# Kernel tuning notes

Hardware: AMD Instinct MI355X
Metric: run time of the kernel (lower is better)

Reference implementation:

```python
import jax, jax.numpy as jnp
import numpy as np

N = 20000      # points
K = 16         # neighbor pairs per query per branch
M = N * K      # total pairs
C = 384        # embed_dim
H = 6          # num_heads
HD = C // H    # head_dim = 64
H1 = H // 2    # cartesian-branch heads
L = 24         # quant_grid_length (window 6.0 / quant 0.25)
Q = 0.25       # quant_size
LS = 24        # quant_grid_length_sphere (120 / 5)
QS = 5.0       # quant_size_sphere
A = 0.05 * 0.25  # exponential_split 'a'
SCALE = HD ** -0.5


def setup_inputs() -> dict:
    key = jax.random.key(0)
    ks = jax.random.split(key, 12)
    s = 0.02
    inp = {}
    inp["query_feats"] = jax.random.normal(ks[0], (N, C), jnp.float32)
    inp["xyz"] = jax.random.uniform(ks[1], (N, 3), jnp.float32, -3.0, 3.0)
    inp["index_0"] = jnp.repeat(jnp.arange(N, dtype=jnp.int32), K)
    inp["index_1"] = jax.random.randint(ks[2], (M,), 0, N, dtype=jnp.int32)
    inp["index_0_sphere"] = jnp.repeat(jnp.arange(N, dtype=jnp.int32), K)
    inp["index_1_sphere"] = jax.random.randint(ks[3], (M,), 0, N, dtype=jnp.int32)
    inp["W_qkv"] = jax.random.normal(ks[4], (C, 3 * C), jnp.float32) * s
    inp["b_qkv"] = jnp.zeros((3 * C,), jnp.float32)
    inp["W_proj"] = jax.random.normal(ks[5], (C, C), jnp.float32) * s
    inp["b_proj"] = jnp.zeros((C,), jnp.float32)
    inp["tq"] = jax.random.normal(ks[6], (2 * L - 1, 3, H1, HD), jnp.float32) * s
    inp["tk"] = jax.random.normal(ks[7], (2 * L - 1, 3, H1, HD), jnp.float32) * s
    inp["tv"] = jax.random.normal(ks[8], (2 * L - 1, 3, H1, HD), jnp.float32) * s
    inp["tq_s"] = jax.random.normal(ks[9], (2 * LS, 3, H - H1, HD), jnp.float32) * s
    inp["tk_s"] = jax.random.normal(ks[10], (2 * LS, 3, H - H1, HD), jnp.float32) * s
    inp["tv_s"] = jax.random.normal(ks[11], (2 * LS, 3, H - H1, HD), jnp.float32) * s
    return inp


def _cart2sphere(xyz):
    x, y, z = xyz[:, 0], xyz[:, 1], xyz[:, 2]
    theta = (jnp.arctan2(y, x) + np.pi) * (180.0 / np.pi)
    beta = jnp.arctan2(jnp.sqrt(x * x + y * y), z) * (180.0 / np.pi)
    r = jnp.sqrt(x * x + y * y + z * z)
    return jnp.stack([theta, beta, r], -1)


def _rel_idx_cart(xyz, i0, i1):
    rel = xyz[i0] - xyz[i1]  # [M,3]
    idx = jnp.floor(rel / Q).astype(jnp.int32) + (L - 1)
    return jnp.clip(idx, 0, 2 * L - 2)


def _rel_idx_sphere(sph, i0, i1):
    rel = sph[i0] - sph[i1]  # [M,3] (theta, beta, r)
    idx01 = jnp.clip(jnp.floor(rel[:, :2] / QS).astype(jnp.int32) + LS, 0, 2 * LS - 1)
    # exponential_split on radial dim
    r = rel[:, 2]
    ra = jnp.abs(r)
    flag = (r >= 0).astype(jnp.float32)
    idx = 2.0 * jnp.floor(jnp.log((ra + 2.0 * A) / A) / np.log(2.0)) - 2.0
    idx = idx + ((3.0 * jnp.exp2(jnp.floor(idx / 2.0)) - 2.0) * A <= ra).astype(jnp.float32)
    idx = idx * (2.0 * flag - 1.0) + (flag - 1.0)
    idx2 = jnp.clip(idx.astype(jnp.int32) + 24, 0, 2 * LS - 1)
    return jnp.concatenate([idx01, idx2[:, None]], 1)


def _branch(q, k, v, i0, i1, rel_idx, Tq, Tk, Tv):
    # q,k,v: [N,h,d]; i0/i1: [M]; rel_idx: [M,3]; tables: [R,3,h,d]
    qg = q[i0]  # [M,h,d]
    kg = k[i1]
    attn = jnp.einsum('mhd,mhd->mh', qg, kg)
    for dim in range(3):
        attn = attn + jnp.einsum('mhd,mhd->mh', qg, Tq[rel_idx[:, dim], dim])
        attn = attn + jnp.einsum('mhd,mhd->mh', kg, Tk[rel_idx[:, dim], dim])
    # segment softmax over queries (i0)
    seg_max = jax.ops.segment_max(attn, i0, num_segments=N)
    ex = jnp.exp(attn - seg_max[i0])
    p = ex / jax.ops.segment_sum(ex, i0, num_segments=N)[i0]  # [M,h]
    vg = v[i1] + Tv[rel_idx[:, 0], 0] + Tv[rel_idx[:, 1], 1] + Tv[rel_idx[:, 2], 2]
    return jax.ops.segment_sum(p[:, :, None] * vg, i0, num_segments=N)  # [N,h,d]


def reference(query_feats, xyz, index_0, index_1, index_0_sphere, index_1_sphere,
              W_qkv, b_qkv, W_proj, b_proj, tq, tk, tv, tq_s, tk_s, tv_s):
    i0 = index_0.astype(jnp.int32)
    i1 = index_1.astype(jnp.int32)
    i0s = index_0_sphere.astype(jnp.int32)
    i1s = index_1_sphere.astype(jnp.int32)
    qkv = (query_feats @ W_qkv + b_qkv).reshape(N, 3, H, HD)
    q = qkv[:, 0] * SCALE
    k = qkv[:, 1]
    v = qkv[:, 2]
    sph = _cart2sphere(xyz)
    ri = _rel_idx_cart(xyz, i0, i1)
    out1 = _branch(q[:, :H1], k[:, :H1], v[:, :H1], i0, i1, ri, tq, tk, tv)
    ri_s = _rel_idx_sphere(sph, i0s, i1s)
    out2 = _branch(q[:, H1:], k[:, H1:], v[:, H1:], i0s, i1s, ri_s, tq_s, tk_s, tv_s)
    x = jnp.concatenate([out1, out2], 1).reshape(N, C)
    return x @ W_proj + b_proj
```

## Files before the change

kernel.cpp:

```cpp
#include <hip/hip_runtime.h>
#include <hip/hip_bf16.h>

namespace {

constexpr int NP   = 20000;
constexpr int CD   = 384;
constexpr int QKVD = 1152;
constexpr int TC   = 47 * 3 * 3 * 64;
constexpr int TS   = 48 * 3 * 3 * 64;

typedef __attribute__((ext_vector_type(8))) short short8;
typedef __attribute__((ext_vector_type(4))) float f32x4;
typedef __attribute__((ext_vector_type(2))) float f32x2;

__device__ inline float f32_atan2(float y, float x) {
  return (float)atan2((double)y, (double)x);
}
__device__ inline float f32_log(float x) {
  return (float)log((double)x);
}

__device__ inline float bfl(unsigned u) {
  union { unsigned u; float f; } c; c.u = u << 16; return c.f;
}
__device__ inline float bfh(unsigned u) {
  union { unsigned u; float f; } c; c.u = u & 0xffff0000u; return c.f;
}
__device__ inline f32x2 up2(unsigned u) {
  f32x2 r;
  r.x = bfl(u);
  r.y = bfh(u);
  return r;
}
__device__ inline unsigned short f2bf(float x) {
  __hip_bfloat16 hb = __float2bfloat16(x);
  unsigned short u; __builtin_memcpy(&u, &hb, 2);
  return u;
}

#if __has_builtin(__builtin_amdgcn_fdot2_f32_bf16)
#define HAVE_BF16_DOT 1
typedef __attribute__((ext_vector_type(2))) __bf16 bf16x2_t;
__device__ inline float dot2bf(unsigned a, unsigned b, float c) {
  bf16x2_t av, bv;
  __builtin_memcpy(&av, &a, 4);
  __builtin_memcpy(&bv, &b, 4);
  return __builtin_amdgcn_fdot2_f32_bf16(av, bv, c, false);
}
#endif

__device__ inline void async16(const void* g, void* l) {
  __builtin_amdgcn_global_load_lds(
      (const __attribute__((address_space(1))) unsigned int*)g,
      (__attribute__((address_space(3))) unsigned int*)l,
      16, 0, 0);
}

__global__ __launch_bounds__(256) void cvt_bf16_k(const float* __restrict__ in,
                                                  unsigned short* __restrict__ out, int n) {
  int i = (blockIdx.x * 256 + threadIdx.x) * 4;
  if (i < n) {
    float4 v = *(const float4*)(in + i);
    ushort4 o;
    o.x = f2bf(v.x); o.y = f2bf(v.y); o.z = f2bf(v.z); o.w = f2bf(v.w);
    *(ushort4*)(out + i) = o;
  }
}

__global__ __launch_bounds__(256) void transpose_cvt_k(const float* __restrict__ in,
                                                       unsigned short* __restrict__ out,
                                                       int R, int Cc) {
  __shared__ float t[32][33];
  int c0 = blockIdx.x * 32, r0 = blockIdx.y * 32;
  int tx = threadIdx.x, ty = threadIdx.y;
  #pragma unroll
  for (int i = 0; i < 32; i += 8)
    t[ty + i][tx] = in[(size_t)(r0 + ty + i) * Cc + (c0 + tx)];
  __syncthreads();
  #pragma unroll
  for (int i = 0; i < 32; i += 8)
    out[(size_t)(c0 + ty + i) * R + (r0 + tx)] = f2bf(t[tx][ty + i]);
}

__global__ __launch_bounds__(256) void prep_k(const float* __restrict__ tq,
                                              const float* __restrict__ tk,
                                              const float* __restrict__ tv,
                                              const float* __restrict__ tqs,
                                              const float* __restrict__ tks,
                                              const float* __restrict__ tvs,
                                              unsigned short* __restrict__ tq_b,
                                              unsigned short* __restrict__ tk_b,
                                              unsigned short* __restrict__ tv_b,
                                              unsigned short* __restrict__ tqs_b,
                                              unsigned short* __restrict__ tks_b,
                                              unsigned short* __restrict__ tvs_b,
                                              const float* __restrict__ xyz,
                                              float* __restrict__ sph) {
  const int y = blockIdx.y;
  const int t = blockIdx.x * 256 + threadIdx.x;
  if (y < 6) {
    const float* in = (y == 0) ? tq : (y == 1) ? tk : (y == 2) ? tv
                    : (y == 3) ? tqs : (y == 4) ? tks : tvs;
    unsigned short* out = (y == 0) ? tq_b : (y == 1) ? tk_b : (y == 2) ? tv_b
                        : (y == 3) ? tqs_b : (y == 4) ? tks_b : tvs_b;
    const int n = (y < 3) ? TC : TS;
    int i = t * 4;
    if (i < n) {
      float4 v = *(const float4*)(in + i);
      ushort4 o;
      o.x = f2bf(v.x); o.y = f2bf(v.y); o.z = f2bf(v.z); o.w = f2bf(v.w);
      *(ushort4*)(out + i) = o;
    }
  } else {
#pragma clang fp contract(off)
    #pragma unroll
    for (int r = 0; r < 4; ++r) {
      int i = t * 4 + r;
      if (i < NP) {
        const float PIF = 3.14159265358979323846f;
        const float R2D = 57.29577951308232f;
        float x = xyz[i * 3 + 0], yy = xyz[i * 3 + 1], z = xyz[i * 3 + 2];
        float sxy = x * x + yy * yy;
        sph[i * 3 + 0] = (f32_atan2(yy, x) + PIF) * R2D;
        sph[i * 3 + 1] = f32_atan2(sqrtf(sxy), z) * R2D;
        sph[i * 3 + 2] = sqrtf(sxy + z * z);
      }
    }
  }
}

template <int MODE>
__global__ __launch_bounds__(256) void gemm_async_k(const short* __restrict__ A,
                                                    const short* __restrict__ BT,
                                                    const float* __restrict__ bias,
                                                    void* __restrict__ Cout,
                                                    int M, int Nn, int K) {
  __shared__ short As[2][128][32];
  __shared__ short Bs[2][128][32];
  const int tid  = threadIdx.x;
  const int m0   = blockIdx.x * 128, n0 = blockIdx.y * 128;
  const int wave = tid >> 6, lane = tid & 63;
  const int wm   = (wave & 1) * 64, wn = (wave >> 1) * 64;
  const int quad = lane >> 4, l16 = lane & 15;
  const int srow = lane >> 2;
  const int scol = (lane & 3) * 8;

  f32x4 acc[4][4] = {};

  auto stage = [&](int buf, int k0) {
    #pragma unroll
    for (int c = 0; c < 2; ++c) {
      const int base = (wave + c * 4) * 16;
      const int gmr = m0 + base + srow;
      if (gmr < M)
        async16(A + (size_t)gmr * K + k0 + scol, &As[buf][base][0]);
      const int gnr = n0 + base + srow;
      if (gnr < Nn)
        async16(BT + (size_t)gnr * K + k0 + scol, &Bs[buf][base][0]);
    }
  };

  stage(0, 0);
  int cur = 0;
  for (int k0 = 0; k0 < K; k0 += 32) {
    __syncthreads();
    if (k0 + 32 < K) stage(cur ^ 1, k0 + 32);
    short8 af[4], bg[4];
    #pragma unroll
    for (int i = 0; i < 4; ++i) af[i] = *(const short8*)&As[cur][wm + i * 16 + l16][quad * 8];
    #pragma unroll
    for (int j = 0; j < 4; ++j) bg[j] = *(const short8*)&Bs[cur][wn + j * 16 + l16][quad * 8];
    #pragma unroll
    for (int i = 0; i < 4; ++i)
      #pragma unroll
      for (int j = 0; j < 4; ++j)
        acc[i][j] = __builtin_amdgcn_mfma_f32_16x16x32_bf16(af[i], bg[j], acc[i][j], 0, 0, 0);
    cur ^= 1;
  }

  #pragma unroll
  for (int i = 0; i < 4; ++i) {
    #pragma unroll
    for (int j = 0; j < 4; ++j) {
      int gn = n0 + wn + j * 16 + l16;
      if (gn >= Nn) continue;
      float bval = bias[gn];
      #pragma unroll
      for (int r = 0; r < 4; ++r) {
        int gm = m0 + wm + i * 16 + quad * 4 + r;
        if (gm < M) {
          float v = acc[i][j][r] + bval;
          if (MODE == 0) {
            if (gn < 384) v *= 0.125f;
            ((unsigned short*)Cout)[(size_t)gm * Nn + gn] = f2bf(v);
          } else {
            ((float*)Cout)[(size_t)gm * Nn + gn] = v;
          }
        }
      }
    }
  }
}

__device__ inline f32x2 dot8_pk(uint4 q, uint4 k, uint4 a0, uint4 a1, uint4 a2,
                                uint4 t0, uint4 t1, uint4 t2, f32x2 acc) {
  const unsigned* qp = &q.x;  const unsigned* kp = &k.x;
  const unsigned* a0p = &a0.x; const unsigned* a1p = &a1.x; const unsigned* a2p = &a2.x;
  const unsigned* t0p = &t0.x; const unsigned* t1p = &t1.x; const unsigned* t2p = &t2.x;
  #pragma unroll
  for (int w2 = 0; w2 < 4; ++w2) {
    f32x2 qf = up2(qp[w2]), kf = up2(kp[w2]);
    f32x2 tqs = up2(a0p[w2]) + up2(a1p[w2]) + up2(a2p[w2]);
    f32x2 tks = up2(t0p[w2]) + up2(t1p[w2]) + up2(t2p[w2]);
    acc += qf * (kf + tqs) + kf * tks;
  }
  return acc;
}

__device__ inline void acc4(f32x2* vc, uint4 vv, uint4 t0, uint4 t1, uint4 t2,
                            float pr) {
  f32x2 prv = {pr, pr};
  vc[0] += prv * (up2(vv.x) + up2(t0.x) + up2(t1.x) + up2(t2.x));
  vc[1] += prv * (up2(vv.y) + up2(t0.y) + up2(t1.y) + up2(t2.y));
  vc[2] += prv * (up2(vv.z) + up2(t0.z) + up2(t1.z) + up2(t2.z));
  vc[3] += prv * (up2(vv.w) + up2(t0.w) + up2(t1.w) + up2(t2.w));
}

__global__ __launch_bounds__(256) void attn3_k(const unsigned short* __restrict__ qkv,
                                               const float* __restrict__ xyz,
                                               const float* __restrict__ sph,
                                               const int* __restrict__ nb_c,
                                               const int* __restrict__ nb_s,
                                               const unsigned short* __restrict__ tq_c,
                                               const unsigned short* __restrict__ tk_c,
                                               const unsigned short* __restrict__ tv_c,
                                               const unsigned short* __restrict__ tq_s,
                                               const unsigned short* __restrict__ tk_s,
                                               const unsigned short* __restrict__ tv_s,
                                               unsigned short* __restrict__ xout) {
  __shared__ int   s_i1 [4][16];
  __shared__ int   s_off[4][16][3];
  __shared__ float s_attn[4][3][16];
  __shared__ float s_p   [4][3][16];

  const int w    = threadIdx.x >> 6;
  const int lane = threadIdx.x & 63;
  const int n    = blockIdx.x * 2 + (w >> 1);
  const int b    = w & 1;

  const unsigned short* tqb = b ? tq_s : tq_c;
  const unsigned short* tkb = b ? tk_s : tk_c;
  const unsigned short* tvb = b ? tv_s : tv_c;

  if (lane < 16) {
#pragma clang fp contract(off)
    const int e = lane;
    if (b == 0) {
      const int i1 = nb_c[n * 16 + e];
      s_i1[w][e] = i1;
      const float rel[3] = {xyz[n * 3 + 0] - xyz[i1 * 3 + 0],
                            xyz[n * 3 + 1] - xyz[i1 * 3 + 1],
                            xyz[n * 3 + 2] - xyz[i1 * 3 + 2]};
      #pragma unroll
      for (int dim = 0; dim < 3; ++dim) {
        int idx = (int)floorf(rel[dim] * 4.0f) + 23;
        idx = min(max(idx, 0), 46);
        s_off[w][e][dim] = (idx * 3 + dim) * 192;
      }
    } else {
      const int i1 = nb_s[n * 16 + e];
      s_i1[w][e] = i1;
      const float d0 = sph[n * 3 + 0] - sph[i1 * 3 + 0];
      const float d1 = sph[n * 3 + 1] - sph[i1 * 3 + 1];
      const float dr = sph[n * 3 + 2] - sph[i1 * 3 + 2];
      int i0a = (int)floorf(d0 / 5.0f) + 24;
      int i1a = (int)floorf(d1 / 5.0f) + 24;
      const float ra = fabsf(dr);
      const float flag = (dr >= 0.0f) ? 1.0f : 0.0f;
      const float t = (ra + 0.025f) / 0.0125f;
      const float wv = f32_log(t) / 0.69314718055994531f;
      float fidx = 2.0f * floorf(wv) - 2.0f;
      fidx += ((3.0f * exp2f(floorf(fidx * 0.5f)) - 2.0f) * 0.0125f <= ra) ? 1.0f : 0.0f;
      fidx = fidx * (2.0f * flag - 1.0f) + (flag - 1.0f);
      int i2a = (int)fidx + 24;
      s_off[w][e][0] = (min(max(i0a, 0), 47) * 3 + 0) * 192;
      s_off[w][e][1] = (min(max(i1a, 0), 47) * 3 + 1) * 192;
      s_off[w][e][2] = (min(max(i2a, 0), 47) * 3 + 2) * 192;
    }
  }

  const int eg = lane >> 2, g = lane & 3;
  const int goff = g * 16;
  {
    const int i1 = s_i1[w][eg];
    const int o0 = s_off[w][eg][0];
    const int o1 = s_off[w][eg][1];
    const int o2 = s_off[w][eg][2];
    const unsigned short* kp = qkv + (size_t)i1 * QKVD + 384 + b * 192 + goff;
    const unsigned short* qp = qkv + (size_t)n * QKVD + b * 192 + goff;
    #pragma unroll
    for (int hh = 0; hh < 3; ++hh) {
      const int ho = hh * 64;
      uint4 kv0 = *(const uint4*)(kp + ho);
      uint4 kv1 = *(const uint4*)(kp + ho + 8);
      uint4 qv0 = *(const uint4*)(qp + ho);
      uint4 qv1 = *(const uint4*)(qp + ho + 8);
      uint4 a00 = *(const uint4*)(tqb + o0 + ho + goff);
      uint4 a01 = *(const uint4*)(tqb + o0 + ho + goff + 8);
      uint4 a10 = *(const uint4*)(tqb + o1 + ho + goff);
      uint4 a11 = *(const uint4*)(tqb + o1 + ho + goff + 8);
      uint4 a20 = *(const uint4*)(tqb + o2 + ho + goff);
      uint4 a21 = *(const uint4*)(tqb + o2 + ho + goff + 8);
      uint4 b00 = *(const uint4*)(tkb + o0 + ho + goff);
      uint4 b01 = *(const uint4*)(tkb + o0 + ho + goff + 8);
      uint4 b10 = *(const uint4*)(tkb + o1 + ho + goff);
      uint4 b11 = *(const uint4*)(tkb + o1 + ho + goff + 8);
      uint4 b20 = *(const uint4*)(tkb + o2 + ho + goff);
      uint4 b21 = *(const uint4*)(tkb + o2 + ho + goff + 8);
      float acc;
#ifdef HAVE_BF16_DOT
      float aqk = 0.0f, aq0 = 0.0f, aq1 = 0.0f, aq2 = 0.0f;
      float ak0 = 0.0f, ak1 = 0.0f, ak2 = 0.0f;
#define DOT7(qd, kd, a0d, a1d, a2d, b0d, b1d, b2d)                         \
      aqk = dot2bf(qd, kd, aqk);  aq0 = dot2bf(qd, a0d, aq0);              \
      aq1 = dot2bf(qd, a1d, aq1); aq2 = dot2bf(qd, a2d, aq2);              \
      ak0 = dot2bf(kd, b0d, ak0); ak1 = dot2bf(kd, b1d, ak1);              \
      ak2 = dot2bf(kd, b2d, ak2);
      DOT7(qv0.x, kv0.x, a00.x, a10.x, a20.x, b00.x, b10.x, b20.x)
      DOT7(qv0.y, kv0.y, a00.y, a10.y, a20.y, b00.y, b10.y, b20.y)
      DOT7(qv0.z, kv0.z, a00.z, a10.z, a20.z, b00.z, b10.z, b20.z)
      DOT7(qv0.w, kv0.w, a00.w, a10.w, a20.w, b00.w, b10.w, b20.w)
      DOT7(qv1.x, kv1.x, a01.x, a11.x, a21.x, b01.x, b11.x, b21.x)
      DOT7(qv1.y, kv1.y, a01.y, a11.y, a21.y, b01.y, b11.y, b21.y)
      DOT7(qv1.z, kv1.z, a01.z, a11.z, a21.z, b01.z, b11.z, b21.z)
      DOT7(qv1.w, kv1.w, a01.w, a11.w, a21.w, b01.w, b11.w, b21.w)
#undef DOT7
      acc = ((aqk + aq0) + (aq1 + aq2)) + ((ak0 + ak1) + ak2);
#else
      f32x2 acc2 = {0.0f, 0.0f};
      acc2 = dot8_pk(qv0, kv0, a00, a10, a20, b00, b10, b20, acc2);
      acc2 = dot8_pk(qv1, kv1, a01, a11, a21, b01, b11, b21, acc2);
      acc = acc2.x + acc2.y;
#endif
      acc += __shfl_xor(acc, 1);
      acc += __shfl_xor(acc, 2);
      if (g == 0) s_attn[w][hh][eg] = acc;
    }
  }

  if (lane < 48) {
    const int hh = lane >> 4, ee = lane & 15;
    float a = s_attn[w][hh][ee];
    float m = a;
    #pragma unroll
    for (int off = 8; off > 0; off >>= 1) m = fmaxf(m, __shfl_xor(m, off));
    float ex = __expf(a - m);
    float s = ex;
    #pragma unroll
    for (int off = 8; off > 0; off >>= 1) s += __shfl_xor(s, off);
    s_p[w][hh][ee] = ex / s;
  }

  {
    const int e8 = lane >> 3;
    const int c  = lane & 7;
    const int offVa = s_i1[w][e8]     * QKVD + 768 + b * 192 + c * 8;
    const int offVb = s_i1[w][e8 + 8] * QKVD + 768 + b * 192 + c * 8;
    const int offA0 = s_off[w][e8][0] + c * 8;
    const int offA1 = s_off[w][e8][1] + c * 8;
    const int offA2 = s_off[w][e8][2] + c * 8;
    const int offB0 = s_off[w][e8 + 8][0] + c * 8;
    const int offB1 = s_off[w][e8 + 8][1] + c * 8;
    const int offB2 = s_off[w][e8 + 8][2] + c * 8;
    #pragma unroll
    for (int hh = 0; hh < 3; ++hh) {
      const int ho = hh * 64;
      f32x2 vc[4] = {{0.f, 0.f}, {0.f, 0.f}, {0.f, 0.f}, {0.f, 0.f}};
      {
        uint4 vv = *(const uint4*)(qkv + offVa + ho);
        uint4 t0 = *(const uint4*)(tvb + offA0 + ho);
        uint4 t1 = *(const uint4*)(tvb + offA1 + ho);
        uint4 t2 = *(const uint4*)(tvb + offA2 + ho);
        acc4(vc, vv, t0, t1, t2, s_p[w][hh][e8]);
      }
      {
        uint4 vv = *(const uint4*)(qkv + offVb + ho);
        uint4 t0 = *(const uint4*)(tvb + offB0 + ho);
        uint4 t1 = *(const uint4*)(tvb + offB1 + ho);
        uint4 t2 = *(const uint4*)(tvb + offB2 + ho);
        acc4(vc, vv, t0, t1, t2, s_p[w][hh][e8 + 8]);
      }
      #pragma unroll
      for (int q4 = 0; q4 < 4; ++q4) {
        #pragma unroll
        for (int off = 8; off <= 32; off <<= 1) {
          vc[q4].x += __shfl_xor(vc[q4].x, off);
          vc[q4].y += __shfl_xor(vc[q4].y, off);
        }
      }
      if (e8 == 0) {
        uint4 o;
        o.x = ((unsigned)f2bf(vc[0].y) << 16) | (unsigned)f2bf(vc[0].x);
        o.y = ((unsigned)f2bf(vc[1].y) << 16) | (unsigned)f2bf(vc[1].x);
        o.z = ((unsigned)f2bf(vc[2].y) << 16) | (unsigned)f2bf(vc[2].x);
        o.w = ((unsigned)f2bf(vc[3].y) << 16) | (unsigned)f2bf(vc[3].x);
        *(uint4*)(xout + (size_t)n * CD + (b * 3 + hh) * 64 + c * 8) = o;
      }
    }
  }
}

}

extern "C" void kernel_launch(void* const* d_in, const int* in_sizes, int n_in,
                              void* d_out, int out_size, void* d_ws, size_t ws_size,
                              hipStream_t stream) {
  const float* qf    = (const float*)d_in[0];
  const float* xyz   = (const float*)d_in[1];
  const int*   i1c   = (const int*)d_in[3];
  const int*   i1s   = (const int*)d_in[5];
  const float* Wqkv  = (const float*)d_in[6];
  const float* bqkv  = (const float*)d_in[7];
  const float* Wproj = (const float*)d_in[8];
  const float* bproj = (const float*)d_in[9];
  const float* tq    = (const float*)d_in[10];
  const float* tk    = (const float*)d_in[11];
  const float* tv    = (const float*)d_in[12];
  const float* tqs   = (const float*)d_in[13];
  const float* tks   = (const float*)d_in[14];
  const float* tvs   = (const float*)d_in[15];

  char* w = (char*)d_ws;
  unsigned short* qf_b   = (unsigned short*)w; w += (size_t)NP * CD * 2;
  unsigned short* wqkvT  = (unsigned short*)w; w += (size_t)QKVD * CD * 2;
  unsigned short* wprojT = (unsigned short*)w; w += (size_t)CD * CD * 2;
  unsigned short* qkv_b  = (unsigned short*)w; w += (size_t)NP * QKVD * 2;
  unsigned short* x_b    = (unsigned short*)w; w += (size_t)NP * CD * 2;
  float*          sph    = (float*)w;          w += (size_t)NP * 3 * 4;
  unsigned short* tq_b   = (unsigned short*)w; w += (size_t)TC * 2;
  unsigned short* tk_b   = (unsigned short*)w; w += (size_t)TC * 2;
  unsigned short* tv_b   = (unsigned short*)w; w += (size_t)TC * 2;
  unsigned short* tqs_b  = (unsigned short*)w; w += (size_t)TS * 2;
  unsigned short* tks_b  = (unsigned short*)w; w += (size_t)TS * 2;
  unsigned short* tvs_b  = (unsigned short*)w;

  cvt_bf16_k<<<(NP * CD / 4 + 255) / 256, 256, 0, stream>>>(qf, qf_b, NP * CD);
  transpose_cvt_k<<<dim3(QKVD / 32, CD / 32), dim3(32, 8), 0, stream>>>(Wqkv, wqkvT, CD, QKVD);
  transpose_cvt_k<<<dim3(CD / 32, CD / 32), dim3(32, 8), 0, stream>>>(Wproj, wprojT, CD, CD);
  prep_k<<<dim3(27, 7), 256, 0, stream>>>(tq, tk, tv, tqs, tks, tvs,
                                          tq_b, tk_b, tv_b, tqs_b, tks_b, tvs_b, xyz, sph);

  gemm_async_k<0><<<dim3((NP + 127) / 128, QKVD / 128), 256, 0, stream>>>(
      (const short*)qf_b, (const short*)wqkvT, bqkv, qkv_b, NP, QKVD, CD);

  attn3_k<<<NP / 2, 256, 0, stream>>>(qkv_b, xyz, sph, i1c, i1s,
                                      tq_b, tk_b, tv_b, tqs_b, tks_b, tvs_b, x_b);

  gemm_async_k<1><<<dim3((NP + 127) / 128, CD / 128), 256, 0, stream>>>(
      (const short*)x_b, (const short*)wprojT, bproj, d_out, NP, CD, CD);
}
```

Before: 310.3 us.

## Merge prep kernels, pipeline GEMM LDS loads, double-buffer attention gathers

Folds the four preprocessing launches (feature cast, two weight transposes, table and sphere prep) into one kernel dispatched by block index, cutting launch overhead. The GEMM drops per-row bounds checks on async LDS loads and replaces __syncthreads with explicit vmcnt waits plus barriers, so the next tile's loads overlap the current MFMAs. The attention kernel hoists the query loads, double-buffers the key/table and value/table gathers across heads with sched barriers, and raises the launch-bounds occupancy hint. Without bounds checks the last GEMM row-tile reads past the end of its input buffers into adjacent workspace, and the extra buffered registers may pressure the occupancy target.

```diff
diff --git a/kernel.cpp b/kernel.cpp
--- a/kernel.cpp
+++ b/kernel.cpp
@@ -8,6 +8,11 @@
 constexpr int QKVD = 1152;
 constexpr int TC   = 47 * 3 * 3 * 64;
 constexpr int TS   = 48 * 3 * 3 * 64;
+
+constexpr int PB0 = NP * CD / 4 / 256;
+constexpr int PB1 = PB0 + (QKVD / 32) * (CD / 32);
+constexpr int PB2 = PB1 + (CD / 32) * (CD / 32);
+constexpr int PB3 = PB2 + 27 * 7;
 
 typedef __attribute__((ext_vector_type(8))) short short8;
 typedef __attribute__((ext_vector_type(4))) float f32x4;
@@ -56,74 +61,87 @@
       16, 0, 0);
 }
 
-__global__ __launch_bounds__(256) void cvt_bf16_k(const float* __restrict__ in,
-                                                  unsigned short* __restrict__ out, int n) {
-  int i = (blockIdx.x * 256 + threadIdx.x) * 4;
-  if (i < n) {
-    float4 v = *(const float4*)(in + i);
+__global__ __launch_bounds__(256) void prep_all_k(const float* __restrict__ qf,
+                                                  unsigned short* __restrict__ qf_b,
+                                                  const float* __restrict__ Wqkv,
+                                                  unsigned short* __restrict__ wqkvT,
+                                                  const float* __restrict__ Wproj,
+                                                  unsigned short* __restrict__ wprojT,
+                                                  const float* __restrict__ tq,
+                                                  const float* __restrict__ tk,
+                                                  const float* __restrict__ tv,
+                                                  const float* __restrict__ tqs,
+                                                  const float* __restrict__ tks,
+                                                  const float* __restrict__ tvs,
+                                                  unsigned short* __restrict__ tq_b,
+                                                  unsigned short* __restrict__ tk_b,
+                                                  unsigned short* __restrict__ tv_b,
+                                                  unsigned short* __restrict__ tqs_b,
+                                                  unsigned short* __restrict__ tks_b,
+                                                  unsigned short* __restrict__ tvs_b,
+                                                  const float* __restrict__ xyz,
+                                                  float* __restrict__ sph) {
+  const int bid = blockIdx.x;
+  const int tid = threadIdx.x;
+  __shared__ float t[32][33];
+
+  if (bid < PB0) {
+    int i = (bid * 256 + tid) * 4;
+    float4 v = *(const float4*)(qf + i);
     ushort4 o;
     o.x = f2bf(v.x); o.y = f2bf(v.y); o.z = f2bf(v.z); o.w = f2bf(v.w);
-    *(ushort4*)(out + i) = o;
-  }
-}
-
-__global__ __launch_bounds__(256) void transpose_cvt_k(const float* __restrict__ in,
-                                                       unsigned short* __restrict__ out,
-                                                       int R, int Cc) {
-  __shared__ float t[32][33];
-  int c0 = blockIdx.x * 32, r0 = blockIdx.y * 32;
-  int tx = threadIdx.x, ty = threadIdx.y;
-  #pragma unroll
-  for (int i = 0; i < 32; i += 8)
-    t[ty + i][tx] = in[(size_t)(r0 + ty + i) * Cc + (c0 + tx)];
-  __syncthreads();
-  #pragma unroll
-  for (int i = 0; i < 32; i += 8)
-    out[(size_t)(c0 + ty + i) * R + (r0 + tx)] = f2bf(t[tx][ty + i]);
-}
-
-__global__ __launch_bounds__(256) void prep_k(const float* __restrict__ tq,
-                                              const float* __restrict__ tk,
-                                              const float* __restrict__ tv,
-                                              const float* __restrict__ tqs,
-                                              const float* __restrict__ tks,
-                                              const float* __restrict__ tvs,
-                                              unsigned short* __restrict__ tq_b,
-                                              unsigned short* __restrict__ tk_b,
-                                              unsigned short* __restrict__ tv_b,
-                                              unsigned short* __restrict__ tqs_b,
-                                              unsigned short* __restrict__ tks_b,
-                                              unsigned short* __restrict__ tvs_b,
-                                              const float* __restrict__ xyz,
-                                              float* __restrict__ sph) {
-  const int y = blockIdx.y;
-  const int t = blockIdx.x * 256 + threadIdx.x;
-  if (y < 6) {
-    const float* in = (y == 0) ? tq : (y == 1) ? tk : (y == 2) ? tv
-                    : (y == 3) ? tqs : (y == 4) ? tks : tvs;
-    unsigned short* out = (y == 0) ? tq_b : (y == 1) ? tk_b : (y == 2) ? tv_b
-                        : (y == 3) ? tqs_b : (y == 4) ? tks_b : tvs_b;
-    const int n = (y < 3) ? TC : TS;
-    int i = t * 4;
-    if (i < n) {
-      float4 v = *(const float4*)(in + i);
-      ushort4 o;
-      o.x = f2bf(v.x); o.y = f2bf(v.y); o.z = f2bf(v.z); o.w = f2bf(v.w);
-      *(ushort4*)(out + i) = o;
-    }
+    *(ushort4*)(qf_b + i) = o;
+  } else if (bid < PB2) {
+    const float* in;
+    unsigned short* out;
+    int R, Cc, bx, by;
+    if (bid < PB1) {
+      in = Wqkv; out = wqkvT; R = CD; Cc = QKVD;
+      int tt = bid - PB0; bx = tt % (QKVD / 32); by = tt / (QKVD / 32);
+    } else {
+      in = Wproj; out = wprojT; R = CD; Cc = CD;
+      int tt = bid - PB1; bx = tt % (CD / 32); by = tt / (CD / 32);
+    }
+    const int c0 = bx * 32, r0 = by * 32;
+    const int tx = tid & 31, ty = tid >> 5;
+    #pragma unroll
+    for (int i = 0; i < 32; i += 8)
+      t[ty + i][tx] = in[(size_t)(r0 + ty + i) * Cc + (c0 + tx)];
+    __syncthreads();
+    #pragma unroll
+    for (int i = 0; i < 32; i += 8)
+      out[(size_t)(c0 + ty + i) * R + (r0 + tx)] = f2bf(t[tx][ty + i]);
   } else {
+    const int tt = bid - PB2;
+    const int bx = tt % 27, y = tt / 27;
+    const int th = bx * 256 + tid;
+    if (y < 6) {
+      const float* in = (y == 0) ? tq : (y == 1) ? tk : (y == 2) ? tv
+                      : (y == 3) ? tqs : (y == 4) ? tks : tvs;
+      unsigned short* out = (y == 0) ? tq_b : (y == 1) ? tk_b : (y == 2) ? tv_b
+                          : (y == 3) ? tqs_b : (y == 4) ? tks_b : tvs_b;
+      const int n = (y < 3) ? TC : TS;
+      int i = th * 4;
+      if (i < n) {
+        float4 v = *(const float4*)(in + i);
+        ushort4 o;
+        o.x = f2bf(v.x); o.y = f2bf(v.y); o.z = f2bf(v.z); o.w = f2bf(v.w);
+        *(ushort4*)(out + i) = o;
+      }
+    } else {
 #pragma clang fp contract(off)
-    #pragma unroll
-    for (int r = 0; r < 4; ++r) {
-      int i = t * 4 + r;
-      if (i < NP) {
-        const float PIF = 3.14159265358979323846f;
-        const float R2D = 57.29577951308232f;
-        float x = xyz[i * 3 + 0], yy = xyz[i * 3 + 1], z = xyz[i * 3 + 2];
-        float sxy = x * x + yy * yy;
-        sph[i * 3 + 0] = (f32_atan2(yy, x) + PIF) * R2D;
-        sph[i * 3 + 1] = f32_atan2(sqrtf(sxy), z) * R2D;
-        sph[i * 3 + 2] = sqrtf(sxy + z * z);
+      #pragma unroll
+      for (int r = 0; r < 4; ++r) {
+        int i = th * 4 + r;
+        if (i < NP) {
+          const float PIF = 3.14159265358979323846f;
+          const float R2D = 57.29577951308232f;
+          float x = xyz[i * 3 + 0], yy = xyz[i * 3 + 1], z = xyz[i * 3 + 2];
+          float sxy = x * x + yy * yy;
+          sph[i * 3 + 0] = (f32_atan2(yy, x) + PIF) * R2D;
+          sph[i * 3 + 1] = f32_atan2(sqrtf(sxy), z) * R2D;
+          sph[i * 3 + 2] = sqrtf(sxy + z * z);
+        }
       }
     }
   }
@@ -151,20 +169,21 @@
     #pragma unroll
     for (int c = 0; c < 2; ++c) {
       const int base = (wave + c * 4) * 16;
-      const int gmr = m0 + base + srow;
-      if (gmr < M)
-        async16(A + (size_t)gmr * K + k0 + scol, &As[buf][base][0]);
-      const int gnr = n0 + base + srow;
-      if (gnr < Nn)
-        async16(BT + (size_t)gnr * K + k0 + scol, &Bs[buf][base][0]);
+      async16(A + (size_t)(m0 + base + srow) * K + k0 + scol, &As[buf][base][0]);
+      async16(BT + (size_t)(n0 + base + srow) * K + k0 + scol, &Bs[buf][base][0]);
     }
   };
 
   stage(0, 0);
   int cur = 0;
   for (int k0 = 0; k0 < K; k0 += 32) {
-    __syncthreads();
-    if (k0 + 32 < K) stage(cur ^ 1, k0 + 32);
+    if (k0 + 32 < K) {
+      stage(cur ^ 1, k0 + 32);
+      asm volatile("s_waitcnt vmcnt(4)" ::: "memory");
+    } else {
+      asm volatile("s_waitcnt vmcnt(0)" ::: "memory");
+    }
+    __builtin_amdgcn_s_barrier();
     short8 af[4], bg[4];
     #pragma unroll
     for (int i = 0; i < 4; ++i) af[i] = *(const short8*)&As[cur][wm + i * 16 + l16][quad * 8];
@@ -175,6 +194,7 @@
       #pragma unroll
       for (int j = 0; j < 4; ++j)
         acc[i][j] = __builtin_amdgcn_mfma_f32_16x16x32_bf16(af[i], bg[j], acc[i][j], 0, 0, 0);
+    __builtin_amdgcn_s_barrier();
     cur ^= 1;
   }
 
@@ -226,18 +246,18 @@
   vc[3] += prv * (up2(vv.w) + up2(t0.w) + up2(t1.w) + up2(t2.w));
 }
 
-__global__ __launch_bounds__(256) void attn3_k(const unsigned short* __restrict__ qkv,
-                                               const float* __restrict__ xyz,
-                                               const float* __restrict__ sph,
-                                               const int* __restrict__ nb_c,
-                                               const int* __restrict__ nb_s,
-                                               const unsigned short* __restrict__ tq_c,
-                                               const unsigned short* __restrict__ tk_c,
-                                               const unsigned short* __restrict__ tv_c,
-                                               const unsigned short* __restrict__ tq_s,
-                                               const unsigned short* __restrict__ tk_s,
-                                               const unsigned short* __restrict__ tv_s,
-                                               unsigned short* __restrict__ xout) {
+__global__ __launch_bounds__(256, 3) void attn3_k(const unsigned short* __restrict__ qkv,
+                                                  const float* __restrict__ xyz,
+                                                  const float* __restrict__ sph,
+                                                  const int* __restrict__ nb_c,
+                                                  const int* __restrict__ nb_s,
+                                                  const unsigned short* __restrict__ tq_c,
+                                                  const unsigned short* __restrict__ tk_c,
+                                                  const unsigned short* __restrict__ tv_c,
+                                                  const unsigned short* __restrict__ tq_s,
+                                                  const unsigned short* __restrict__ tk_s,
+                                                  const unsigned short* __restrict__ tv_s,
+                                                  unsigned short* __restrict__ xout) {
   __shared__ int   s_i1 [4][16];
   __shared__ int   s_off[4][16][3];
   __shared__ float s_attn[4][3][16];
@@ -251,6 +271,16 @@
   const unsigned short* tqb = b ? tq_s : tq_c;
   const unsigned short* tkb = b ? tk_s : tk_c;
   const unsigned short* tvb = b ? tv_s : tv_c;
+
+  const int eg = lane >> 2, g = lane & 3;
+  const int goff = g * 16;
+  const unsigned short* qp = qkv + (size_t)n * QKVD + b * 192 + goff;
+  uint4 qv[3][2];
+  #pragma unroll
+  for (int hh = 0; hh < 3; ++hh) {
+    qv[hh][0] = *(const uint4*)(qp + hh * 64);
+    qv[hh][1] = *(const uint4*)(qp + hh * 64 + 8);
+  }
 
   if (lane < 16) {
 #pragma clang fp contract(off)
@@ -289,63 +319,76 @@
     }
   }
 
-  const int eg = lane >> 2, g = lane & 3;
-  const int goff = g * 16;
   {
     const int i1 = s_i1[w][eg];
-    const int o0 = s_off[w][eg][0];
-    const int o1 = s_off[w][eg][1];
-    const int o2 = s_off[w][eg][2];
+    const int o0 = s_off[w][eg][0] + goff;
+    const int o1 = s_off[w][eg][1] + goff;
+    const int o2 = s_off[w][eg][2] + goff;
     const unsigned short* kp = qkv + (size_t)i1 * QKVD + 384 + b * 192 + goff;
-    const unsigned short* qp = qkv + (size_t)n * QKVD + b * 192 + goff;
+
+    uint4 kc[2][2], ta[2][6], tb[2][6];
+#define LDH(buf, ho) do {                                                    \
+    kc[buf][0] = *(const uint4*)(kp + (ho));                                 \
+    kc[buf][1] = *(const uint4*)(kp + (ho) + 8);                             \
+    ta[buf][0] = *(const uint4*)(tqb + o0 + (ho));                           \
+    ta[buf][1] = *(const uint4*)(tqb + o0 + (ho) + 8);                       \
+    ta[buf][2] = *(const uint4*)(tqb + o1 + (ho));                           \
+    ta[buf][3] = *(const uint4*)(tqb + o1 + (ho) + 8);                       \
+    ta[buf][4] = *(const uint4*)(tqb + o2 + (ho));                           \
+    ta[buf][5] = *(const uint4*)(tqb + o2 + (ho) + 8);                       \
+    tb[buf][0] = *(const uint4*)(tkb + o0 + (ho));                           \
+    tb[buf][1] = *(const uint4*)(tkb + o0 + (ho) + 8);                       \
+    tb[buf][2] = *(const uint4*)(tkb + o1 + (ho));                           \
+    tb[buf][3] = *(const uint4*)(tkb + o1 + (ho) + 8);                       \
+    tb[buf][4] = *(const uint4*)(tkb + o2 + (ho));                           \
+    tb[buf][5] = *(const uint4*)(tkb + o2 + (ho) + 8);                       \
+  } while (0)
+
+    LDH(0, 0);
     #pragma unroll
     for (int hh = 0; hh < 3; ++hh) {
-      const int ho = hh * 64;
-      uint4 kv0 = *(const uint4*)(kp + ho);
-      uint4 kv1 = *(const uint4*)(kp + ho + 8);
-      uint4 qv0 = *(const uint4*)(qp + ho);
-      uint4 qv1 = *(const uint4*)(qp + ho + 8);
-      uint4 a00 = *(const uint4*)(tqb + o0 + ho + goff);
-      uint4 a01 = *(const uint4*)(tqb + o0 + ho + goff + 8);
-      uint4 a10 = *(const uint4*)(tqb + o1 + ho + goff);
-      uint4 a11 = *(const uint4*)(tqb + o1 + ho + goff + 8);
-      uint4 a20 = *(const uint4*)(tqb + o2 + ho + goff);
-      uint4 a21 = *(const uint4*)(tqb + o2 + ho + goff + 8);
-      uint4 b00 = *(const uint4*)(tkb + o0 + ho + goff);
-      uint4 b01 = *(const uint4*)(tkb + o0 + ho + goff + 8);
-      uint4 b10 = *(const uint4*)(tkb + o1 + ho + goff);
-      uint4 b11 = *(const uint4*)(tkb + o1 + ho + goff + 8);
-      uint4 b20 = *(const uint4*)(tkb + o2 + ho + goff);
-      uint4 b21 = *(const uint4*)(tkb + o2 + ho + goff + 8);
+      const int cur = hh & 1;
+      if (hh < 2) LDH(cur ^ 1, (hh + 1) * 64);
+      __builtin_amdgcn_sched_barrier(0);
       float acc;
 #ifdef HAVE_BF16_DOT
       float aqk = 0.0f, aq0 = 0.0f, aq1 = 0.0f, aq2 = 0.0f;
       float ak0 = 0.0f, ak1 = 0.0f, ak2 = 0.0f;
-#define DOT7(qd, kd, a0d, a1d, a2d, b0d, b1d, b2d)                         \
-      aqk = dot2bf(qd, kd, aqk);  aq0 = dot2bf(qd, a0d, aq0);              \
-      aq1 = dot2bf(qd, a1d, aq1); aq2 = dot2bf(qd, a2d, aq2);              \
-      ak0 = dot2bf(kd, b0d, ak0); ak1 = dot2bf(kd, b1d, ak1);              \
-      ak2 = dot2bf(kd, b2d, ak2);
-      DOT7(qv0.x, kv0.x, a00.x, a10.x, a20.x, b00.x, b10.x, b20.x)
-      DOT7(qv0.y, kv0.y, a00.y, a10.y, a20.y, b00.y, b10.y, b20.y)
-      DOT7(qv0.z, kv0.z, a00.z, a10.z, a20.z, b00.z, b10.z, b20.z)
-      DOT7(qv0.w, kv0.w, a00.w, a10.w, a20.w, b00.w, b10.w, b20.w)
-      DOT7(qv1.x, kv1.x, a01.x, a11.x, a21.x, b01.x, b11.x, b21.x)
-      DOT7(qv1.y, kv1.y, a01.y, a11.y, a21.y, b01.y, b11.y, b21.y)
-      DOT7(qv1.z, kv1.z, a01.z, a11.z, a21.z, b01.z, b11.z, b21.z)
-      DOT7(qv1.w, kv1.w, a01.w, a11.w, a21.w, b01.w, b11.w, b21.w)
-#undef DOT7
+      #pragma unroll
+      for (int u = 0; u < 2; ++u) {
+        const unsigned* qd = (const unsigned*)&qv[hh][u];
+        const unsigned* kd = (const unsigned*)&kc[cur][u];
+        const unsigned* a0 = (const unsigned*)&ta[cur][u];
+        const unsigned* a1 = (const unsigned*)&ta[cur][2 + u];
+        const unsigned* a2 = (const unsigned*)&ta[cur][4 + u];
+        const unsigned* b0 = (const unsigned*)&tb[cur][u];
+        const unsigned* b1 = (const unsigned*)&tb[cur][2 + u];
+        const unsigned* b2 = (const unsigned*)&tb[cur][4 + u];
+        #pragma unroll
+        for (int d = 0; d < 4; ++d) {
+          aqk = dot2bf(qd[d], kd[d], aqk);
+          aq0 = dot2bf(qd[d], a0[d], aq0);
+          aq1 = dot2bf(qd[d], a1[d], aq1);
+          aq2 = dot2bf(qd[d], a2[d], aq2);
+          ak0 = dot2bf(kd[d], b0[d], ak0);
+          ak1 = dot2bf(kd[d], b1[d], ak1);
+          ak2 = dot2bf(kd[d], b2[d], ak2);
+        }
+      }
       acc = ((aqk + aq0) + (aq1 + aq2)) + ((ak0 + ak1) + ak2);
 #else
       f32x2 acc2 = {0.0f, 0.0f};
-      acc2 = dot8_pk(qv0, kv0, a00, a10, a20, b00, b10, b20, acc2);
-      acc2 = dot8_pk(qv1, kv1, a01, a11, a21, b01, b11, b21, acc2);
+      acc2 = dot8_pk(qv[hh][0], kc[cur][0], ta[cur][0], ta[cur][2], ta[cur][4],
+                     tb[cur][0], tb[cur][2], tb[cur][4], acc2);
+      acc2 = dot8_pk(qv[hh][1], kc[cur][1], ta[cur][1], ta[cur][3], ta[cur][5],
+                     tb[cur][1], tb[cur][3], tb[cur][5], acc2);
       acc = acc2.x + acc2.y;
 #endif
       acc += __shfl_xor(acc, 1);
       acc += __shfl_xor(acc, 2);
       if (g == 0) s_attn[w][hh][eg] = acc;
     }
+#undef LDH
   }
 
   if (lane < 48) {
@@ -372,24 +415,28 @@
     const int offB0 = s_off[w][e8 + 8][0] + c * 8;
     const int offB1 = s_off[w][e8 + 8][1] + c * 8;
     const int offB2 = s_off[w][e8 + 8][2] + c * 8;
+
+    uint4 vA[2], tA0[2], tA1[2], tA2[2], vB[2], tB0[2], tB1[2], tB2[2];
+#define LDV(buf, ho) do {                                                    \
+    vA [buf] = *(const uint4*)(qkv + offVa + (ho));                          \
+    tA0[buf] = *(const uint4*)(tvb + offA0 + (ho));                          \
+    tA1[buf] = *(const uint4*)(tvb + offA1 + (ho));                          \
+    tA2[buf] = *(const uint4*)(tvb + offA2 + (ho));                          \
+    vB [buf] = *(const uint4*)(qkv + offVb + (ho));                          \
+    tB0[buf] = *(const uint4*)(tvb + offB0 + (ho));                          \
+    tB1[buf] = *(const uint4*)(tvb + offB1 + (ho));                          \
+    tB2[buf] = *(const uint4*)(tvb + offB2 + (ho));                          \
+  } while (0)
+
+    LDV(0, 0);
     #pragma unroll
     for (int hh = 0; hh < 3; ++hh) {
-      const int ho = hh * 64;
+      const int cur = hh & 1;
+      if (hh < 2) LDV(cur ^ 1, (hh + 1) * 64);
+      __builtin_amdgcn_sched_barrier(0);
       f32x2 vc[4] = {{0.f, 0.f}, {0.f, 0.f}, {0.f, 0.f}, {0.f, 0.f}};
-      {
-        uint4 vv = *(const uint4*)(qkv + offVa + ho);
-        uint4 t0 = *(const uint4*)(tvb + offA0 + ho);
-        uint4 t1 = *(const uint4*)(tvb + offA1 + ho);
-        uint4 t2 = *(const uint4*)(tvb + offA2 + ho);
-        acc4(vc, vv, t0, t1, t2, s_p[w][hh][e8]);
-      }
-      {
-        uint4 vv = *(const uint4*)(qkv + offVb + ho);
-        uint4 t0 = *(const uint4*)(tvb + offB0 + ho);
-        uint4 t1 = *(const uint4*)(tvb + offB1 + ho);
-        uint4 t2 = *(const uint4*)(tvb + offB2 + ho);
-        acc4(vc, vv, t0, t1, t2, s_p[w][hh][e8 + 8]);
-      }
+      acc4(vc, vA[cur], tA0[cur], tA1[cur], tA2[cur], s_p[w][hh][e8]);
+      acc4(vc, vB[cur], tB0[cur], tB1[cur], tB2[cur], s_p[w][hh][e8 + 8]);
       #pragma unroll
       for (int q4 = 0; q4 < 4; ++q4) {
         #pragma unroll
@@ -407,6 +454,7 @@
         *(uint4*)(xout + (size_t)n * CD + (b * 3 + hh) * 64 + c * 8) = o;
       }
     }
+#undef LDV
   }
 }
 
@@ -444,11 +492,10 @@
   unsigned short* tks_b  = (unsigned short*)w; w += (size_t)TS * 2;
   unsigned short* tvs_b  = (unsigned short*)w;
 
-  cvt_bf16_k<<<(NP * CD / 4 + 255) / 256, 256, 0, stream>>>(qf, qf_b, NP * CD);
-  transpose_cvt_k<<<dim3(QKVD / 32, CD / 32), dim3(32, 8), 0, stream>>>(Wqkv, wqkvT, CD, QKVD);
-  transpose_cvt_k<<<dim3(CD / 32, CD / 32), dim3(32, 8), 0, stream>>>(Wproj, wprojT, CD, CD);
-  prep_k<<<dim3(27, 7), 256, 0, stream>>>(tq, tk, tv, tqs, tks, tvs,
-                                          tq_b, tk_b, tv_b, tqs_b, tks_b, tvs_b, xyz, sph);
+  prep_all_k<<<PB3, 256, 0, stream>>>(qf, qf_b, Wqkv, wqkvT, Wproj, wprojT,
+                                      tq, tk, tv, tqs, tks, tvs,
+                                      tq_b, tk_b, tv_b, tqs_b, tks_b, tvs_b,
+                                      xyz, sph);
 
   gemm_async_k<0><<<dim3((NP + 127) / 128, QKVD / 128), 256, 0, stream>>>(
       (const short*)qf_b, (const short*)wqkvT, bqkv, qkv_b, NP, QKVD, CD);
```

Result: no change. 313.1 us (+0.9%).
